# Performance work log

Hardware: AMD Instinct MI355X
Metric: run time of the kernel (lower is better)

## Reference

```python
import jax, jax.numpy as jnp
import numpy as np

STATE_DIM = 256
ACT_LEN = 128
INPUT_DIM = STATE_DIM + 2 * ACT_LEN
B_SZ, T = 32, 2048
SLOPE = 0.01


def leaky(x):
    return jnp.where(x < 0, SLOPE * x, x)


def inv_leaky(x):
    return jnp.where(x < 0, x / SLOPE, x)


def _lin_init(key, out_d, in_d):
    k1, k2 = jax.random.split(key)
    bound = 1.0 / np.sqrt(in_d)
    W = jax.random.uniform(k1, (out_d, in_d), minval=-bound, maxval=bound, dtype=jnp.float32)
    b = jax.random.uniform(k2, (out_d,), minval=-bound, maxval=bound, dtype=jnp.float32)
    return W, b


def setup_inputs() -> dict:
    key = jax.random.key(0)
    ks = jax.random.split(key, 8)
    padded_input = jax.random.normal(ks[0], (B_SZ, T, INPUT_DIM), dtype=jnp.float32)
    We1, be1 = _lin_init(ks[1], STATE_DIM, STATE_DIM)
    We2, be2 = _lin_init(ks[2], STATE_DIM, STATE_DIM)
    A_W, A_b = _lin_init(ks[3], STATE_DIM, STATE_DIM)
    B_W, B_b = _lin_init(ks[4], STATE_DIM, ACT_LEN)
    Wd1, bd1 = _lin_init(ks[5], STATE_DIM, STATE_DIM)
    Wd2, bd2 = _lin_init(ks[6], STATE_DIM, STATE_DIM)
    return {"padded_input": padded_input, "We1": We1, "be1": be1, "We2": We2, "be2": be2,
            "A_W": A_W, "A_b": A_b, "B_W": B_W, "B_b": B_b,
            "Wd1": Wd1, "bd1": bd1, "Wd2": Wd2, "bd2": bd2}


def reference(padded_input, We1, be1, We2, be2, A_W, A_b, B_W, B_b, Wd1, bd1, Wd2, bd2):
    x_t = padded_input[:, :, :STATE_DIM]                      # [B,T,D]
    u_t = padded_input[:, :, STATE_DIM:STATE_DIM + ACT_LEN]   # [B,T,A]
    # encoder: (Linear + LeakyReLU) x 2
    z = leaky(jnp.einsum('btd,ed->bte', x_t, We1) + be1)
    z = leaky(jnp.einsum('btd,ed->bte', z, We2) + be2)
    # recurrence z_{t} uses encoded state only at t=0 (reset_probability=0, nwarmup=0)
    Bu = jnp.einsum('bta,da->btd', u_t, B_W) + B_b            # [B,T,D], precomputed
    z0 = z[:, 0, :]                                           # [B,D]

    def step(carry, bu_t):
        out = jnp.einsum('bd,ed->be', carry, A_W) + A_b + bu_t
        return out, out

    _, z1 = jax.lax.scan(step, z0, jnp.swapaxes(Bu, 0, 1))    # z1: [T,B,D]
    z1 = jnp.swapaxes(z1, 0, 1)                               # [B,T,D]
    # decoder: (InverseLeakyReLU + Linear) x 2
    y = jnp.einsum('btd,ed->bte', inv_leaky(z1), Wd1) + bd1
    y = jnp.einsum('btd,ed->bte', inv_leaky(y), Wd2) + bd2
    return y
```

## Files before the change

kernel.cpp:

```cpp
#include <hip/hip_runtime.h>

#define D256 256
#define ALEN 128
#define INDIM 512
#define BSZ 32
#define TLEN 2048
#define CHL 32
#define NCH 64

typedef __attribute__((ext_vector_type(8))) short short8;
typedef __attribute__((ext_vector_type(4))) float f32x4;
typedef __attribute__((ext_vector_type(8))) unsigned short u16x8;

__device__ __forceinline__ float leakyf(float x)  { return x < 0.f ? 0.01f * x : x; }
__device__ __forceinline__ float ileakyf(float x) { return x < 0.f ? x * 100.0f : x; }

__device__ __forceinline__ unsigned short f2bf(float f) {
  unsigned int x = __float_as_uint(f);
  unsigned int r = x + 0x7FFFu + ((x >> 16) & 1u);
  return (unsigned short)(r >> 16);
}

__device__ __forceinline__ float bf2f(unsigned short u) {
  return __uint_as_float(((unsigned int)u) << 16);
}

__device__ __forceinline__ void gload16(const void* g, const void* l) {
  __builtin_amdgcn_global_load_lds(
      (const __attribute__((address_space(1))) unsigned int*)g,
      (__attribute__((address_space(3))) unsigned int*)l, 16, 0, 0);
}

template <int CTRL>
__device__ __forceinline__ float dpp_addf(float x) {
  return x + __int_as_float(__builtin_amdgcn_update_dpp(
                 0, __float_as_int(x), CTRL, 0xF, 0xF, true));
}
__device__ __forceinline__ void red8(float4& s) {
  s.x = dpp_addf<0xB1>(s.x); s.y = dpp_addf<0xB1>(s.y);
  s.z = dpp_addf<0xB1>(s.z); s.w = dpp_addf<0xB1>(s.w);
  s.x = dpp_addf<0x4E>(s.x); s.y = dpp_addf<0x4E>(s.y);
  s.z = dpp_addf<0x4E>(s.z); s.w = dpp_addf<0x4E>(s.w);
  s.x = dpp_addf<0x141>(s.x); s.y = dpp_addf<0x141>(s.y);
  s.z = dpp_addf<0x141>(s.z); s.w = dpp_addf<0x141>(s.w);
}

__global__ __launch_bounds__(256) void gemm_mfma(
    const unsigned short* __restrict__ In, int K,
    const unsigned short* __restrict__ W,
    const float* __restrict__ bias1, const float* __restrict__ bias2,
    int ileaky_act, int out_bf16, void* __restrict__ Outp) {
  __shared__ char lds[16384];
  __shared__ float ldsF[32][132];
  const int tid = threadIdx.x;
  const int lane = tid & 63, w = tid >> 6;
  const int m0 = blockIdx.x * 128, n0 = blockIdx.y * 128;
  const int wm = (w & 1) * 64, wn = (w >> 1) * 64;
  const int quad = lane >> 4, l16 = lane & 15;

  f32x4 acc[4][4];
#pragma unroll
  for (int i = 0; i < 4; ++i)
#pragma unroll
    for (int j = 0; j < 4; ++j) acc[i][j] = {0.f, 0.f, 0.f, 0.f};

  for (int kb = 0; kb < K; kb += 32) {
    __syncthreads();
#pragma unroll
    for (int q = 0; q < 2; ++q) {
      const int id = (w * 2 + q) * 64 + lane;
      const int row = id >> 2, ch = id & 3;
      gload16(In + (size_t)(m0 + row) * K + kb + ch * 8,
              lds + (w * 2 + q) * 1024);
      gload16(W + (size_t)(n0 + row) * K + kb + ch * 8,
              lds + 8192 + (w * 2 + q) * 1024);
    }
    __syncthreads();

    short8 af[4], bf[4];
#pragma unroll
    for (int i = 0; i < 4; ++i) {
      af[i] = *(const short8*)(lds + ((wm + i * 16 + l16) * 64 + quad * 16));
      bf[i] = *(const short8*)(lds + 8192 + ((wn + i * 16 + l16) * 64 + quad * 16));
    }
#pragma unroll
    for (int i = 0; i < 4; ++i)
#pragma unroll
      for (int j = 0; j < 4; ++j)
        acc[i][j] = __builtin_amdgcn_mfma_f32_16x16x32_bf16(af[i], bf[j], acc[i][j], 0, 0, 0);
  }

  const int lrow = tid >> 3, c0 = (tid & 7) * 16;
#pragma unroll
  for (int p = 0; p < 4; ++p) {
    if ((w & 1) == (p >> 1)) {
      const int ib = 2 * (p & 1);
#pragma unroll
      for (int ii = 0; ii < 2; ++ii)
#pragma unroll
        for (int j = 0; j < 4; ++j)
#pragma unroll
          for (int r = 0; r < 4; ++r)
            ldsF[ii * 16 + quad * 4 + r][wn + j * 16 + l16] = acc[ib + ii][j][r];
    }
    __syncthreads();
    const int m = m0 + p * 32 + lrow;
    const int nb = n0 + c0;
    float v[16];
#pragma unroll
    for (int k = 0; k < 4; ++k) {
      const float4 b1 = *(const float4*)&bias1[nb + 4 * k];
#pragma unroll
      for (int c = 0; c < 4; ++c) v[4 * k + c] = ldsF[lrow][c0 + 4 * k + c] + ((const float*)&b1)[c];
    }
    if (bias2) {
#pragma unroll
      for (int k = 0; k < 4; ++k) {
        const float4 b2 = *(const float4*)&bias2[nb + 4 * k];
#pragma unroll
        for (int c = 0; c < 4; ++c) v[4 * k + c] += ((const float*)&b2)[c];
      }
    }
    if (ileaky_act) {
#pragma unroll
      for (int c = 0; c < 16; ++c) v[c] = ileakyf(v[c]);
    }
    if (out_bf16) {
      unsigned short* op = (unsigned short*)Outp + (size_t)m * 256 + nb;
#pragma unroll
      for (int h = 0; h < 2; ++h) {
        u16x8 ov;
#pragma unroll
        for (int c = 0; c < 8; ++c) ov[c] = f2bf(v[h * 8 + c]);
        *(u16x8*)(op + h * 8) = ov;
      }
    } else {
      float* op = (float*)Outp + (size_t)m * 256 + nb;
#pragma unroll
      for (int k = 0; k < 4; ++k)
        *(float4*)(op + 4 * k) = make_float4(v[4 * k], v[4 * k + 1], v[4 * k + 2], v[4 * k + 3]);
    }
    __syncthreads();
  }
}

__global__ __launch_bounds__(256) void gemm_corr(
    const unsigned short* __restrict__ Eb, const unsigned short* __restrict__ Mb,
    unsigned short* w1 ) {
  __shared__ char lds[16384];
  __shared__ float ldsF[32][132];
  const int tid = threadIdx.x;
  const int lane = tid & 63, w = tid >> 6;
  const int m0 = blockIdx.x * 128, n0 = blockIdx.y * 128;
  const int wm = (w & 1) * 64, wn = (w >> 1) * 64;
  const int quad = lane >> 4, l16 = lane & 15;

  f32x4 acc[4][4];
#pragma unroll
  for (int i = 0; i < 4; ++i)
#pragma unroll
    for (int j = 0; j < 4; ++j) acc[i][j] = {0.f, 0.f, 0.f, 0.f};

  for (int kb = 0; kb < 256; kb += 32) {
    __syncthreads();
#pragma unroll
    for (int q = 0; q < 2; ++q) {
      const int id = (w * 2 + q) * 64 + lane;
      const int row = id >> 2, ch = id & 3;
      gload16(Eb + (size_t)(m0 + row) * 256 + kb + ch * 8,
              lds + (w * 2 + q) * 1024);
      gload16(Mb + (size_t)(n0 + row) * 256 + kb + ch * 8,
              lds + 8192 + (w * 2 + q) * 1024);
    }
    __syncthreads();

    short8 af[4], bf[4];
#pragma unroll
    for (int i = 0; i < 4; ++i) {
      af[i] = *(const short8*)(lds + ((wm + i * 16 + l16) * 64 + quad * 16));
      bf[i] = *(const short8*)(lds + 8192 + ((wn + i * 16 + l16) * 64 + quad * 16));
    }
#pragma unroll
    for (int i = 0; i < 4; ++i)
#pragma unroll
      for (int j = 0; j < 4; ++j)
        acc[i][j] = __builtin_amdgcn_mfma_f32_16x16x32_bf16(af[i], bf[j], acc[i][j], 0, 0, 0);
  }

  const int lrow = tid >> 3, c0 = (tid & 7) * 16;
#pragma unroll
  for (int p = 0; p < 4; ++p) {
    if ((w & 1) == (p >> 1)) {
      const int ib = 2 * (p & 1);
#pragma unroll
      for (int ii = 0; ii < 2; ++ii)
#pragma unroll
        for (int j = 0; j < 4; ++j)
#pragma unroll
          for (int r = 0; r < 4; ++r)
            ldsF[ii * 16 + quad * 4 + r][wn + j * 16 + l16] = acc[ib + ii][j][r];
    }
    __syncthreads();
    const int m = m0 + p * 32 + lrow;
    const int kk = m >> 5, bb = m & 31;
    const int nb = n0 + c0;
    const int jj = nb >> 8, e = nb & 255;
    const size_t addr = ((size_t)bb * TLEN + (size_t)kk * CHL + jj) * 256 + e;
#pragma unroll
    for (int h = 0; h < 2; ++h) {
      const u16x8 dv = *(const u16x8*)&w1[addr + h * 8];
      u16x8 ov;
#pragma unroll
      for (int c = 0; c < 8; ++c) {
        float v = ldsF[lrow][c0 + h * 8 + c] + bf2f(dv[c]);
        ov[c] = f2bf(ileakyf(v));
      }
      *(u16x8*)&w1[addr + h * 8] = ov;
    }
    __syncthreads();
  }
}

__global__ __launch_bounds__(256) void gemm_pow(
    const float* __restrict__ P, const float* __restrict__ XTb,
    float* __restrict__ OutS, float* __restrict__ OutST,
    unsigned short* __restrict__ OutSb) {
  __shared__ float a_lds[64][40];
  __shared__ float b_lds[64][40];
  const size_t zo = (size_t)blockIdx.z << 16;
  const float* XT = XTb + zo;
  const int tid = threadIdx.x;
  const int tm = tid >> 4, tn = tid & 15;
  const int m0 = blockIdx.x * 64, n0 = blockIdx.y * 64;
  float acc[4][4];
#pragma unroll
  for (int i = 0; i < 4; ++i)
#pragma unroll
    for (int j = 0; j < 4; ++j) acc[i][j] = 0.f;

  for (int kb = 0; kb < 256; kb += 32) {
    __syncthreads();
#pragma unroll
    for (int q = 0; q < 2; ++q) {
      const int slot = q * 256 + tid;
      const int row = slot >> 3, s4 = slot & 7;
      *(float4*)&a_lds[row][s4 * 4] = *(const float4*)&P[(size_t)(m0 + row) * 256 + kb + s4 * 4];
      *(float4*)&b_lds[row][s4 * 4] = *(const float4*)&XT[(size_t)(n0 + row) * 256 + kb + s4 * 4];
    }
    __syncthreads();
#pragma unroll
    for (int k4 = 0; k4 < 8; ++k4) {
      float4 a4[4], b4[4];
#pragma unroll
      for (int i = 0; i < 4; ++i) a4[i] = *(const float4*)&a_lds[tm * 4 + i][k4 * 4];
#pragma unroll
      for (int j = 0; j < 4; ++j) b4[j] = *(const float4*)&b_lds[tn * 4 + j][k4 * 4];
#pragma unroll
      for (int i = 0; i < 4; ++i)
#pragma unroll
        for (int j = 0; j < 4; ++j)
          acc[i][j] += a4[i].x * b4[j].x + a4[i].y * b4[j].y +
                       a4[i].z * b4[j].z + a4[i].w * b4[j].w;
    }
  }
  float* Out = OutS + zo;
  float* OutT = OutST + zo;
  unsigned short* Ob = OutSb + zo;
#pragma unroll
  for (int i = 0; i < 4; ++i) {
    const int m = m0 + tm * 4 + i;
    float4 v = make_float4(acc[i][0], acc[i][1], acc[i][2], acc[i][3]);
    *(float4*)&Out[(size_t)m * 256 + n0 + tn * 4] = v;
    *(ushort4*)&Ob[(size_t)m * 256 + n0 + tn * 4] =
        make_ushort4(f2bf(v.x), f2bf(v.y), f2bf(v.z), f2bf(v.w));
#pragma unroll
    for (int j = 0; j < 4; ++j)
      OutT[(size_t)(n0 + tn * 4 + j) * 256 + m] = acc[i][j];
  }
}

__global__ __launch_bounds__(256) void prep_kernel(
    const float* __restrict__ in, const float* __restrict__ We1,
    const float* __restrict__ be1, const float* __restrict__ We2,
    const float* __restrict__ be2, const float* __restrict__ A_W,
    const float* __restrict__ B_W, const float* __restrict__ Wd1,
    const float* __restrict__ Wd2, float* __restrict__ AT0,
    unsigned short* __restrict__ Ab0, float* __restrict__ z0,
    unsigned short* __restrict__ BWb, unsigned short* __restrict__ Wd1b,
    unsigned short* __restrict__ Wd2b) {
  __shared__ float sm[1056];
  const int tid = threadIdx.x;
  const int blk = blockIdx.x;
  if (blk < 64) {
    const int bx = (blk & 7) * 32, by = (blk >> 3) * 32;
    const int lx = tid & 31, ly = tid >> 5;
#pragma unroll
    for (int i = 0; i < 4; ++i) {
      const float v = A_W[(size_t)(by + ly + 8 * i) * 256 + bx + lx];
      sm[(ly + 8 * i) * 33 + lx] = v;
      Ab0[(size_t)(by + ly + 8 * i) * 256 + bx + lx] = f2bf(v);
    }
    __syncthreads();
#pragma unroll
    for (int i = 0; i < 4; ++i)
      AT0[(size_t)(bx + ly + 8 * i) * 256 + by + lx] = sm[lx * 33 + ly + 8 * i];
  } else if (blk < 96) {
    const int b = blk - 64, e = tid;
    float* xb = sm;
    float* h1 = sm + 256;
    xb[e] = in[(size_t)b * TLEN * INDIM + e];
    __syncthreads();
    float acc = be1[e];
    const float4* w = (const float4*)(We1 + (size_t)e * 256);
#pragma unroll 8
    for (int d4 = 0; d4 < 64; ++d4) {
      float4 wv = w[d4];
      acc += wv.x * xb[4 * d4] + wv.y * xb[4 * d4 + 1] + wv.z * xb[4 * d4 + 2] + wv.w * xb[4 * d4 + 3];
    }
    h1[e] = leakyf(acc);
    __syncthreads();
    float a2 = be2[e];
    w = (const float4*)(We2 + (size_t)e * 256);
#pragma unroll 8
    for (int d4 = 0; d4 < 64; ++d4) {
      float4 wv = w[d4];
      a2 += wv.x * h1[4 * d4] + wv.y * h1[4 * d4 + 1] + wv.z * h1[4 * d4 + 2] + wv.w * h1[4 * d4 + 3];
    }
    z0[(size_t)b * 256 + e] = leakyf(a2);
  } else {
    const float* src;
    unsigned short* dst;
    int i4;
    if (blk < 128)      { src = B_W; dst = BWb;  i4 = (blk - 96) * 256 + tid; }
    else if (blk < 192) { src = Wd1; dst = Wd1b; i4 = (blk - 128) * 256 + tid; }
    else                { src = Wd2; dst = Wd2b; i4 = (blk - 192) * 256 + tid; }
    float4 v = *(const float4*)&src[(size_t)i4 * 4];
    *(ushort4*)&dst[(size_t)i4 * 4] =
        make_ushort4(f2bf(v.x), f2bf(v.y), f2bf(v.z), f2bf(v.w));
  }
}

__global__ __launch_bounds__(256) void extract_u(const float* __restrict__ in,
                                                 unsigned short* __restrict__ ubuf) {
  const int gid = blockIdx.x * 256 + threadIdx.x;
  const int row = gid >> 5;
  const int c = (gid & 31) * 4;
  float4 v = *(const float4*)&in[(size_t)row * INDIM + 256 + c];
  *(ushort4*)&ubuf[(size_t)row * 128 + c] =
      make_ushort4(f2bf(v.x), f2bf(v.y), f2bf(v.z), f2bf(v.w));
}

__global__ __launch_bounds__(512, 2) void phase_kernel(
    const float* __restrict__ AW, const float* __restrict__ Cbuf,
    float* __restrict__ Lend, unsigned short* __restrict__ dout) {
  const int tid = threadIdx.x;
  const int w = tid >> 6;
  const int lane = tid & 63;
  const int dg = lane & 7;
  const int le = lane >> 3;
  const int e0 = w * 32 + le * 4;
  const int d0 = dg * 32;
  const int rho0 = blockIdx.x << 3;
  const int k = rho0 >> 5;
  const int b = (rho0 & 31) + dg;
  const int rho = rho0 + dg;

  __shared__ __align__(16) float carry[2][8][292];

  float4 Ar[4][8];
#pragma unroll
  for (int i = 0; i < 4; ++i)
#pragma unroll
    for (int k4 = 0; k4 < 8; ++k4)
      Ar[i][k4] = *(const float4*)&AW[(size_t)(e0 + i) * 256 + d0 + k4 * 4];

  float4 cur = make_float4(0.f, 0.f, 0.f, 0.f);
  const int epad = e0 + ((e0 >> 5) << 2);
  *(float4*)&carry[0][dg][epad] = cur;
  __syncthreads();

  const float4* crow = (const float4*)(Cbuf + ((size_t)b * TLEN + (size_t)k * CHL) * 256 + e0);
  ushort4* wrow = (ushort4*)(dout + ((size_t)b * TLEN + (size_t)k * CHL) * 256 + e0);

  int buf = 0;
  for (int j = 0; j < CHL; ++j) {
    const float4 cj = *crow;
    crow += 64;
    float4 nxt = make_float4(0.f, 0.f, 0.f, 0.f);
#pragma unroll
    for (int r = 0; r < 8; ++r) {
      float4 s = make_float4(0.f, 0.f, 0.f, 0.f);
#pragma unroll
      for (int k4 = 0; k4 < 8; ++k4) {
        const float4 cv = *(const float4*)&carry[buf][r][dg * 36 + k4 * 4];
        s.x += Ar[0][k4].x * cv.x + Ar[0][k4].y * cv.y + Ar[0][k4].z * cv.z + Ar[0][k4].w * cv.w;
        s.y += Ar[1][k4].x * cv.x + Ar[1][k4].y * cv.y + Ar[1][k4].z * cv.z + Ar[1][k4].w * cv.w;
        s.z += Ar[2][k4].x * cv.x + Ar[2][k4].y * cv.y + Ar[2][k4].z * cv.z + Ar[2][k4].w * cv.w;
        s.w += Ar[3][k4].x * cv.x + Ar[3][k4].y * cv.y + Ar[3][k4].z * cv.z + Ar[3][k4].w * cv.w;
      }
      red8(s);
      if (dg == r) nxt = s;
    }
    cur = make_float4(nxt.x + cj.x, nxt.y + cj.y, nxt.z + cj.z, nxt.w + cj.w);
    buf ^= 1;
    *(float4*)&carry[buf][dg][epad] = cur;
    *wrow = make_ushort4(f2bf(cur.x), f2bf(cur.y), f2bf(cur.z), f2bf(cur.w));
    wrow += 64;
    __syncthreads();
  }
  *(float4*)&Lend[(size_t)rho * 256 + e0] = cur;
}

__global__ __launch_bounds__(512, 2) void boundary_kernel(
    const float* __restrict__ P, const float* __restrict__ z0,
    const float* __restrict__ Lend, unsigned short* __restrict__ Eb) {
  const int tid = threadIdx.x;
  const int w = tid >> 6;
  const int lane = tid & 63;
  const int dg = lane & 7;
  const int le = lane >> 3;
  const int e0 = w * 32 + le * 4;
  const int d0 = dg * 32;
  const int b = blockIdx.x;

  __shared__ __align__(16) float Ec[292];

  float4 Pr[4][8];
#pragma unroll
  for (int i = 0; i < 4; ++i)
#pragma unroll
    for (int k4 = 0; k4 < 8; ++k4)
      Pr[i][k4] = *(const float4*)&P[(size_t)(e0 + i) * 256 + d0 + k4 * 4];

  float4 cur = *(const float4*)&z0[(size_t)b * 256 + e0];
  const int epad = e0 + ((e0 >> 5) << 2);
  if (dg == 0) *(float4*)&Ec[epad] = cur;
  __syncthreads();

  for (int k = 0; k < NCH; ++k) {
    const float4 lv = *(const float4*)&Lend[((size_t)k * BSZ + b) * 256 + e0];
    if (dg == 0)
      *(ushort4*)&Eb[((size_t)k * BSZ + b) * 256 + e0] =
          make_ushort4(f2bf(cur.x), f2bf(cur.y), f2bf(cur.z), f2bf(cur.w));

    float4 s = make_float4(0.f, 0.f, 0.f, 0.f);
#pragma unroll
    for (int k4 = 0; k4 < 8; ++k4) {
      const float4 cv = *(const float4*)&Ec[dg * 36 + k4 * 4];
      s.x += Pr[0][k4].x * cv.x + Pr[0][k4].y * cv.y + Pr[0][k4].z * cv.z + Pr[0][k4].w * cv.w;
      s.y += Pr[1][k4].x * cv.x + Pr[1][k4].y * cv.y + Pr[1][k4].z * cv.z + Pr[1][k4].w * cv.w;
      s.z += Pr[2][k4].x * cv.x + Pr[2][k4].y * cv.y + Pr[2][k4].z * cv.z + Pr[2][k4].w * cv.w;
      s.w += Pr[3][k4].x * cv.x + Pr[3][k4].y * cv.y + Pr[3][k4].z * cv.z + Pr[3][k4].w * cv.w;
    }
    red8(s);
    cur = make_float4(s.x + lv.x, s.y + lv.y, s.z + lv.z, s.w + lv.w);
    __syncthreads();
    if (dg == 0) *(float4*)&Ec[epad] = cur;
    __syncthreads();
  }
}

extern "C" void kernel_launch(void* const* d_in, const int* in_sizes, int n_in,
                              void* d_out, int out_size, void* d_ws, size_t ws_size,
                              hipStream_t stream) {
  const float* in  = (const float*)d_in[0];
  const float* We1 = (const float*)d_in[1];
  const float* be1 = (const float*)d_in[2];
  const float* We2 = (const float*)d_in[3];
  const float* be2 = (const float*)d_in[4];
  const float* A_W = (const float*)d_in[5];
  const float* A_b = (const float*)d_in[6];
  const float* B_W = (const float*)d_in[7];
  const float* B_b = (const float*)d_in[8];
  const float* Wd1 = (const float*)d_in[9];
  const float* bd1 = (const float*)d_in[10];
  const float* Wd2 = (const float*)d_in[11];
  const float* bd2 = (const float*)d_in[12];
  float* out = (float*)d_out;

  float* ws     = (float*)d_ws;
  float* Cbuf   = ws;
  float* Mstack = Cbuf + 16777216;
  float* z0     = Mstack + 2097152;
  float* Lend   = z0 + 8192;
  unsigned short* Mstackb = (unsigned short*)(Lend + 524288);
  unsigned short* Eb   = Mstackb + 2097152;
  unsigned short* BWb  = Eb + 524288;
  unsigned short* Wd1b = BWb + 32768;
  unsigned short* Wd2b = Wd1b + 65536;
  float* MstackT = Cbuf;

  unsigned short* ubuf = (unsigned short*)d_out;
  unsigned short* w1   = ubuf + 8388608;
  unsigned short* w2   = (unsigned short*)Cbuf;

  prep_kernel<<<256, 256, 0, stream>>>(in, We1, be1, We2, be2, A_W, B_W, Wd1,
                                       Wd2, MstackT, Mstackb, z0, BWb, Wd1b, Wd2b);

  gemm_pow<<<dim3(4, 4, 1),  256, 0, stream>>>(A_W,                 MstackT, Mstack + 1 * 65536,  MstackT + 1 * 65536,  Mstackb + 1 * 65536);
  gemm_pow<<<dim3(4, 4, 2),  256, 0, stream>>>(Mstack + 1 * 65536,  MstackT, Mstack + 2 * 65536,  MstackT + 2 * 65536,  Mstackb + 2 * 65536);
  gemm_pow<<<dim3(4, 4, 4),  256, 0, stream>>>(Mstack + 3 * 65536,  MstackT, Mstack + 4 * 65536,  MstackT + 4 * 65536,  Mstackb + 4 * 65536);
  gemm_pow<<<dim3(4, 4, 8),  256, 0, stream>>>(Mstack + 7 * 65536,  MstackT, Mstack + 8 * 65536,  MstackT + 8 * 65536,  Mstackb + 8 * 65536);
  gemm_pow<<<dim3(4, 4, 16), 256, 0, stream>>>(Mstack + 15 * 65536, MstackT, Mstack + 16 * 65536, MstackT + 16 * 65536, Mstackb + 16 * 65536);

  extract_u<<<8192, 256, 0, stream>>>(in, ubuf);

  gemm_mfma<<<dim3(512, 2), 256, 0, stream>>>(ubuf, ALEN, BWb, A_b, B_b, 0, 0, Cbuf);

  phase_kernel<<<256, 512, 0, stream>>>(A_W, Cbuf, Lend, w1);
  boundary_kernel<<<32, 512, 0, stream>>>(Mstack + 31 * 65536, z0, Lend, Eb);
  gemm_corr<<<dim3(16, 64), 256, 0, stream>>>(Eb, Mstackb, w1);

  gemm_mfma<<<dim3(512, 2), 256, 0, stream>>>(w1, D256, Wd1b, bd1, nullptr, 1, 1, w2);
  gemm_mfma<<<dim3(512, 2), 256, 0, stream>>>(w2, D256, Wd2b, bd2, nullptr, 0, 0, out);
}
```

Baseline: 652.3 us.

## Halve scan chunk length, process two batch groups per block, fold u-extract into prep

Chunk length for the parallel linear-recurrence scan drops from 32 to 16, giving 128 chunks. Each phase_kernel block now advances two groups of 8 sequences per step so the grid stays at 256 blocks, and the serial chain per block is halved. This needs only matrix powers up to A^16, so one gemm_pow launch goes away and the boundary and correction stages are resized to match. The extract_u work moves into extra blocks of prep_kernel to save a launch, at the cost of more boundary states and more correction-GEMM work.

New measurement: 676.7 us. +3.7%, slower.

```diff
diff --git a/kernel.cpp b/kernel.cpp
--- a/kernel.cpp
+++ b/kernel.cpp
@@ -5,8 +5,8 @@
 #define INDIM 512
 #define BSZ 32
 #define TLEN 2048
-#define CHL 32
-#define NCH 64
+#define CHL 16
+#define NCH 128
 
 typedef __attribute__((ext_vector_type(8))) short short8;
 typedef __attribute__((ext_vector_type(4))) float f32x4;
@@ -287,10 +287,19 @@
     const float* __restrict__ Wd2, float* __restrict__ AT0,
     unsigned short* __restrict__ Ab0, float* __restrict__ z0,
     unsigned short* __restrict__ BWb, unsigned short* __restrict__ Wd1b,
-    unsigned short* __restrict__ Wd2b) {
+    unsigned short* __restrict__ Wd2b, unsigned short* __restrict__ ubuf) {
   __shared__ float sm[1056];
   const int tid = threadIdx.x;
   const int blk = blockIdx.x;
+  if (blk >= 256) {
+    const int gid = (blk - 256) * 256 + tid;
+    const int row = gid >> 5;
+    const int c = (gid & 31) * 4;
+    float4 v = *(const float4*)&in[(size_t)row * INDIM + 256 + c];
+    *(ushort4*)&ubuf[(size_t)row * 128 + c] =
+        make_ushort4(f2bf(v.x), f2bf(v.y), f2bf(v.z), f2bf(v.w));
+    return;
+  }
   if (blk < 64) {
     const int bx = (blk & 7) * 32, by = (blk >> 3) * 32;
     const int lx = tid & 31, ly = tid >> 5;
@@ -340,16 +349,6 @@
   }
 }
 
-__global__ __launch_bounds__(256) void extract_u(const float* __restrict__ in,
-                                                 unsigned short* __restrict__ ubuf) {
-  const int gid = blockIdx.x * 256 + threadIdx.x;
-  const int row = gid >> 5;
-  const int c = (gid & 31) * 4;
-  float4 v = *(const float4*)&in[(size_t)row * INDIM + 256 + c];
-  *(ushort4*)&ubuf[(size_t)row * 128 + c] =
-      make_ushort4(f2bf(v.x), f2bf(v.y), f2bf(v.z), f2bf(v.w));
-}
-
 __global__ __launch_bounds__(512, 2) void phase_kernel(
     const float* __restrict__ AW, const float* __restrict__ Cbuf,
     float* __restrict__ Lend, unsigned short* __restrict__ dout) {
@@ -360,12 +359,15 @@
   const int le = lane >> 3;
   const int e0 = w * 32 + le * 4;
   const int d0 = dg * 32;
-  const int rho0 = blockIdx.x << 3;
+  const int rho0 = blockIdx.x << 4;
   const int k = rho0 >> 5;
-  const int b = (rho0 & 31) + dg;
-  const int rho = rho0 + dg;
-
-  __shared__ __align__(16) float carry[2][8][292];
+  const int b0 = rho0 & 31;
+  const int bA = b0 + dg;
+  const int bB = b0 + 8 + dg;
+  const int rhoA = rho0 + dg;
+  const int rhoB = rho0 + 8 + dg;
+
+  __shared__ __align__(16) float carry[2][2][8][292];
 
   float4 Ar[4][8];
 #pragma unroll
@@ -374,41 +376,66 @@
     for (int k4 = 0; k4 < 8; ++k4)
       Ar[i][k4] = *(const float4*)&AW[(size_t)(e0 + i) * 256 + d0 + k4 * 4];
 
-  float4 cur = make_float4(0.f, 0.f, 0.f, 0.f);
   const int epad = e0 + ((e0 >> 5) << 2);
-  *(float4*)&carry[0][dg][epad] = cur;
+  const float4 fz = make_float4(0.f, 0.f, 0.f, 0.f);
+  *(float4*)&carry[0][0][dg][epad] = fz;
+  *(float4*)&carry[0][1][dg][epad] = fz;
   __syncthreads();
 
-  const float4* crow = (const float4*)(Cbuf + ((size_t)b * TLEN + (size_t)k * CHL) * 256 + e0);
-  ushort4* wrow = (ushort4*)(dout + ((size_t)b * TLEN + (size_t)k * CHL) * 256 + e0);
+  const float4* crowA = (const float4*)(Cbuf + ((size_t)bA * TLEN + (size_t)k * CHL) * 256 + e0);
+  const float4* crowB = (const float4*)(Cbuf + ((size_t)bB * TLEN + (size_t)k * CHL) * 256 + e0);
+  ushort4* wrowA = (ushort4*)(dout + ((size_t)bA * TLEN + (size_t)k * CHL) * 256 + e0);
+  ushort4* wrowB = (ushort4*)(dout + ((size_t)bB * TLEN + (size_t)k * CHL) * 256 + e0);
 
   int buf = 0;
   for (int j = 0; j < CHL; ++j) {
-    const float4 cj = *crow;
-    crow += 64;
-    float4 nxt = make_float4(0.f, 0.f, 0.f, 0.f);
+    const float4 cjA = *crowA;  crowA += 64;
+    const float4 cjB = *crowB;  crowB += 64;
 #pragma unroll
     for (int r = 0; r < 8; ++r) {
       float4 s = make_float4(0.f, 0.f, 0.f, 0.f);
 #pragma unroll
       for (int k4 = 0; k4 < 8; ++k4) {
-        const float4 cv = *(const float4*)&carry[buf][r][dg * 36 + k4 * 4];
+        const float4 cv = *(const float4*)&carry[buf][0][r][dg * 36 + k4 * 4];
         s.x += Ar[0][k4].x * cv.x + Ar[0][k4].y * cv.y + Ar[0][k4].z * cv.z + Ar[0][k4].w * cv.w;
         s.y += Ar[1][k4].x * cv.x + Ar[1][k4].y * cv.y + Ar[1][k4].z * cv.z + Ar[1][k4].w * cv.w;
         s.z += Ar[2][k4].x * cv.x + Ar[2][k4].y * cv.y + Ar[2][k4].z * cv.z + Ar[2][k4].w * cv.w;
         s.w += Ar[3][k4].x * cv.x + Ar[3][k4].y * cv.y + Ar[3][k4].z * cv.z + Ar[3][k4].w * cv.w;
       }
       red8(s);
-      if (dg == r) nxt = s;
-    }
-    cur = make_float4(nxt.x + cj.x, nxt.y + cj.y, nxt.z + cj.z, nxt.w + cj.w);
+      if (dg == r) {
+        const float4 nv = make_float4(s.x + cjA.x, s.y + cjA.y, s.z + cjA.z, s.w + cjA.w);
+        *(float4*)&carry[buf ^ 1][0][dg][epad] = nv;
+        *wrowA = make_ushort4(f2bf(nv.x), f2bf(nv.y), f2bf(nv.z), f2bf(nv.w));
+      }
+    }
+    wrowA += 64;
+#pragma unroll
+    for (int r = 0; r < 8; ++r) {
+      float4 s = make_float4(0.f, 0.f, 0.f, 0.f);
+#pragma unroll
+      for (int k4 = 0; k4 < 8; ++k4) {
+        const float4 cv = *(const float4*)&carry[buf][1][r][dg * 36 + k4 * 4];
+        s.x += Ar[0][k4].x * cv.x + Ar[0][k4].y * cv.y + Ar[0][k4].z * cv.z + Ar[0][k4].w * cv.w;
+        s.y += Ar[1][k4].x * cv.x + Ar[1][k4].y * cv.y + Ar[1][k4].z * cv.z + Ar[1][k4].w * cv.w;
+        s.z += Ar[2][k4].x * cv.x + Ar[2][k4].y * cv.y + Ar[2][k4].z * cv.z + Ar[2][k4].w * cv.w;
+        s.w += Ar[3][k4].x * cv.x + Ar[3][k4].y * cv.y + Ar[3][k4].z * cv.z + Ar[3][k4].w * cv.w;
+      }
+      red8(s);
+      if (dg == r) {
+        const float4 nv = make_float4(s.x + cjB.x, s.y + cjB.y, s.z + cjB.z, s.w + cjB.w);
+        *(float4*)&carry[buf ^ 1][1][dg][epad] = nv;
+        *wrowB = make_ushort4(f2bf(nv.x), f2bf(nv.y), f2bf(nv.z), f2bf(nv.w));
+      }
+    }
+    wrowB += 64;
     buf ^= 1;
-    *(float4*)&carry[buf][dg][epad] = cur;
-    *wrow = make_ushort4(f2bf(cur.x), f2bf(cur.y), f2bf(cur.z), f2bf(cur.w));
-    wrow += 64;
-    __syncthreads();
-  }
-  *(float4*)&Lend[(size_t)rho * 256 + e0] = cur;
+    __syncthreads();
+  }
+  const float4 lA = *(const float4*)&carry[buf][0][dg][epad];
+  const float4 lB = *(const float4*)&carry[buf][1][dg][epad];
+  *(float4*)&Lend[(size_t)rhoA * 256 + e0] = lA;
+  *(float4*)&Lend[(size_t)rhoB * 256 + e0] = lB;
 }
 
 __global__ __launch_bounds__(512, 2) void boundary_kernel(
@@ -481,11 +508,11 @@
   float* ws     = (float*)d_ws;
   float* Cbuf   = ws;
   float* Mstack = Cbuf + 16777216;
-  float* z0     = Mstack + 2097152;
+  float* z0     = Mstack + 1048576;
   float* Lend   = z0 + 8192;
-  unsigned short* Mstackb = (unsigned short*)(Lend + 524288);
-  unsigned short* Eb   = Mstackb + 2097152;
-  unsigned short* BWb  = Eb + 524288;
+  unsigned short* Mstackb = (unsigned short*)(Lend + 1048576);
+  unsigned short* Eb   = Mstackb + 1048576;
+  unsigned short* BWb  = Eb + 1048576;
   unsigned short* Wd1b = BWb + 32768;
   unsigned short* Wd2b = Wd1b + 65536;
   float* MstackT = Cbuf;
@@ -494,22 +521,20 @@
   unsigned short* w1   = ubuf + 8388608;
   unsigned short* w2   = (unsigned short*)Cbuf;
 
-  prep_kernel<<<256, 256, 0, stream>>>(in, We1, be1, We2, be2, A_W, B_W, Wd1,
-                                       Wd2, MstackT, Mstackb, z0, BWb, Wd1b, Wd2b);
-
-  gemm_pow<<<dim3(4, 4, 1),  256, 0, stream>>>(A_W,                 MstackT, Mstack + 1 * 65536,  MstackT + 1 * 65536,  Mstackb + 1 * 65536);
-  gemm_pow<<<dim3(4, 4, 2),  256, 0, stream>>>(Mstack + 1 * 65536,  MstackT, Mstack + 2 * 65536,  MstackT + 2 * 65536,  Mstackb + 2 * 65536);
-  gemm_pow<<<dim3(4, 4, 4),  256, 0, stream>>>(Mstack + 3 * 65536,  MstackT, Mstack + 4 * 65536,  MstackT + 4 * 65536,  Mstackb + 4 * 65536);
-  gemm_pow<<<dim3(4, 4, 8),  256, 0, stream>>>(Mstack + 7 * 65536,  MstackT, Mstack + 8 * 65536,  MstackT + 8 * 65536,  Mstackb + 8 * 65536);
-  gemm_pow<<<dim3(4, 4, 16), 256, 0, stream>>>(Mstack + 15 * 65536, MstackT, Mstack + 16 * 65536, MstackT + 16 * 65536, Mstackb + 16 * 65536);
-
-  extract_u<<<8192, 256, 0, stream>>>(in, ubuf);
+  prep_kernel<<<8448, 256, 0, stream>>>(in, We1, be1, We2, be2, A_W, B_W, Wd1,
+                                        Wd2, MstackT, Mstackb, z0, BWb, Wd1b,
+                                        Wd2b, ubuf);
+
+  gemm_pow<<<dim3(4, 4, 1), 256, 0, stream>>>(A_W,                MstackT, Mstack + 1 * 65536, MstackT + 1 * 65536, Mstackb + 1 * 65536);
+  gemm_pow<<<dim3(4, 4, 2), 256, 0, stream>>>(Mstack + 1 * 65536, MstackT, Mstack + 2 * 65536, MstackT + 2 * 65536, Mstackb + 2 * 65536);
+  gemm_pow<<<dim3(4, 4, 4), 256, 0, stream>>>(Mstack + 3 * 65536, MstackT, Mstack + 4 * 65536, MstackT + 4 * 65536, Mstackb + 4 * 65536);
+  gemm_pow<<<dim3(4, 4, 8), 256, 0, stream>>>(Mstack + 7 * 65536, MstackT, Mstack + 8 * 65536, MstackT + 8 * 65536, Mstackb + 8 * 65536);
 
   gemm_mfma<<<dim3(512, 2), 256, 0, stream>>>(ubuf, ALEN, BWb, A_b, B_b, 0, 0, Cbuf);
 
   phase_kernel<<<256, 512, 0, stream>>>(A_W, Cbuf, Lend, w1);
-  boundary_kernel<<<32, 512, 0, stream>>>(Mstack + 31 * 65536, z0, Lend, Eb);
-  gemm_corr<<<dim3(16, 64), 256, 0, stream>>>(Eb, Mstackb, w1);
+  boundary_kernel<<<32, 512, 0, stream>>>(Mstack + 15 * 65536, z0, Lend, Eb);
+  gemm_corr<<<dim3(32, 32), 256, 0, stream>>>(Eb, Mstackb, w1);
 
   gemm_mfma<<<dim3(512, 2), 256, 0, stream>>>(w1, D256, Wd1b, bd1, nullptr, 1, 1, w2);
   gemm_mfma<<<dim3(512, 2), 256, 0, stream>>>(w2, D256, Wd2b, bd2, nullptr, 0, 0, out);
```
